# Performance work log

Hardware: AMD Instinct MI355X
Metric: run time of the kernel (lower is better)

Reference implementation:

```python
import jax, jax.numpy as jnp
import numpy as np

B, S, C, HD = 2, 4096, 2048, 128
H = C // HD  # 16 heads
EPS = 1.1920929e-07  # torch RMSNorm default eps for float32 (finfo.eps)


def _make_rope(seq_len, head_dim):
    # Standard RoPE 2x2 rotation matrices: [1, S, 1, head_dim//2, 2, 2]
    half = head_dim // 2
    freqs = 1.0 / (10000.0 ** (np.arange(0, half, dtype=np.float32) / half))
    ang = np.arange(seq_len, dtype=np.float32)[:, None] * freqs[None, :]  # [S, half]
    cos, sin = np.cos(ang), np.sin(ang)
    rot = np.stack([np.stack([cos, -sin], axis=-1),
                    np.stack([sin, cos], axis=-1)], axis=-2)  # [S, half, 2, 2]
    return jnp.asarray(rot[None, :, None])  # [1, S, 1, half, 2, 2]


def setup_inputs() -> dict:
    key = jax.random.key(0)
    ks = jax.random.split(key, 9)
    sc = 1.0 / np.sqrt(C)
    return {
        "x": jax.random.normal(ks[0], (B, S, C), jnp.float32),
        "rope": _make_rope(S, HD),
        "wq": jax.random.normal(ks[1], (C, C), jnp.float32) * sc,
        "bq": jax.random.normal(ks[2], (C,), jnp.float32) * 0.01,
        "wk": jax.random.normal(ks[3], (C, C), jnp.float32) * sc,
        "bk": jax.random.normal(ks[4], (C,), jnp.float32) * 0.01,
        "wv": jax.random.normal(ks[5], (C, C), jnp.float32) * sc,
        "bv": jax.random.normal(ks[6], (C,), jnp.float32) * 0.01,
        "q_norm_w": jnp.ones((HD,), jnp.float32),
        "k_norm_w": jnp.ones((HD,), jnp.float32),
    }


def _rmsnorm(t, w):
    t32 = t.astype(jnp.float32)
    inv = jax.lax.rsqrt(jnp.mean(t32 * t32, axis=-1, keepdims=True) + EPS)
    return (t32 * inv * w).astype(t.dtype)


def _apply_rotary(t, rope):
    # t: [B, S, H, HD] -> pairs [B, S, H, HD//2, 1, 2]; rope: [1, S, 1, HD//2, 2, 2]
    t32 = t.reshape(*t.shape[:-1], HD // 2, 1, 2).astype(jnp.float32)
    out = (rope * t32).sum(axis=-1)  # [B, S, H, HD//2, 2]
    return out.reshape(t.shape).astype(t.dtype)


def reference(x, rope, wq, bq, wk, bk, wv, bv, q_norm_w, k_norm_w):
    # QKV projections (torch Linear: x @ W^T + b)
    q = (jnp.einsum('bsc,oc->bso', x, wq) + bq).reshape(B, S, H, HD)
    k = (jnp.einsum('bsc,oc->bso', x, wk) + bk).reshape(B, S, H, HD)
    v = (jnp.einsum('bsc,oc->bso', x, wv) + bv).reshape(B, S, H, HD)
    # Per-head RMSNorm on q, k (in float32, cast back), then rotary
    q = _apply_rotary(_rmsnorm(q, q_norm_w), rope)
    k = _apply_rotary(_rmsnorm(k, k_norm_w), rope)
    return (q, k, v)
```

## Files before the change

kernel.cpp:

```cpp
#include <hip/hip_runtime.h>


#define M_DIM 8192
#define N_DIM 6144
#define K_DIM 2048
#define NKT 32
#define EPS_RMS 1.1920929e-07f

typedef __bf16 bf16x8 __attribute__((ext_vector_type(8)));
typedef float f32x4 __attribute__((ext_vector_type(4)));

__device__ __forceinline__ void gload16(const void* g, void* l) {
  __builtin_amdgcn_global_load_lds(
      (const __attribute__((address_space(1))) unsigned int*)g,
      (__attribute__((address_space(3))) unsigned int*)l, 16, 0, 0);
}

__device__ __forceinline__ unsigned short f2bf(float f) {
  union { float f; unsigned u; } x; x.f = f;
  unsigned r = x.u + 0x7FFFu + ((x.u >> 16) & 1u);
  return (unsigned short)(r >> 16);
}

__global__ void __launch_bounds__(256) cvt_all(
    const float* __restrict__ x, const float* __restrict__ wq,
    const float* __restrict__ wk, const float* __restrict__ wv,
    unsigned short* __restrict__ xbf, unsigned short* __restrict__ wbf) {
  const int nx4 = M_DIM * K_DIM / 4;
  const int nw4 = K_DIM * K_DIM / 4;
  const int tot = nx4 + 3 * nw4;
  int i = blockIdx.x * blockDim.x + threadIdx.x;
  const int stride = gridDim.x * blockDim.x;
  for (; i < tot; i += stride) {
    const float* s;
    unsigned short* d;
    int j;
    if (i < nx4) { s = x; d = xbf; j = i; }
    else {
      const int k = i - nx4;
      const int sel = k / nw4;
      j = k - sel * nw4;
      s = sel == 0 ? wq : (sel == 1 ? wk : wv);
      d = wbf + (size_t)sel * K_DIM * K_DIM;
    }
    const float4 v = reinterpret_cast<const float4*>(s)[j];
    ushort4 o;
    o.x = f2bf(v.x); o.y = f2bf(v.y); o.z = f2bf(v.z); o.w = f2bf(v.w);
    reinterpret_cast<ushort4*>(d)[j] = o;
  }
}

#define LDS4(ARR, BASE, OFF) (*(const f32x4*)((const char*)(ARR) + (BASE) + (OFF)))

#define MFMA_PH(MH, NH)                                                              \
  {                                                                                  \
    _Pragma("unroll")                                                                \
    for (int mf4 = 0; mf4 < 4; ++mf4) {                                              \
      _Pragma("unroll")                                                              \
      for (int nf2 = 0; nf2 < 2; ++nf2) {                                            \
        f32x4& c = acc[(MH) * 4 + mf4][(NH) * 2 + nf2];                              \
        c = __builtin_amdgcn_mfma_f32_16x16x32_bf16(                                 \
            __builtin_bit_cast(bf16x8, Af[mf4][0]),                                  \
            __builtin_bit_cast(bf16x8, Bf[NH][nf2][0]), c, 0, 0, 0);                 \
        c = __builtin_amdgcn_mfma_f32_16x16x32_bf16(                                 \
            __builtin_bit_cast(bf16x8, Af[mf4][1]),                                  \
            __builtin_bit_cast(bf16x8, Bf[NH][nf2][1]), c, 0, 0, 0);                 \
      }                                                                              \
    }                                                                                \
  }

#define FENCE asm volatile("" ::: "memory")

__global__ void __launch_bounds__(512, 2) gemm_fused(
    const unsigned short* __restrict__ xbf, const unsigned short* __restrict__ wbf,
    const float* __restrict__ rope,
    const float* __restrict__ bq, const float* __restrict__ bk, const float* __restrict__ bv,
    const float* __restrict__ qnw, const float* __restrict__ knw,
    float* __restrict__ dout) {
  const int id = blockIdx.x;
  const int xcd = id & 7;
  const int jb = id >> 3;
  const int bm = (xcd << 2) | (jb & 3);
  const int bn = jb >> 2;
  const int m0 = bm << 8, n0 = bn << 8;
  const int tid = threadIdx.x;
  const int w = tid >> 6, l = tid & 63;
  const int l15 = l & 15, lhi = l >> 4;
  const int wr = w >> 2, wc = w & 3;

  __shared__ __align__(16) unsigned short As[32768];
  __shared__ __align__(16) unsigned short Bs[32768];

  const int srow = tid >> 3;
  const int schunk = (tid & 7) ^ (srow & 7);
  const unsigned short* aSrc = xbf + ((size_t)(m0 + srow) << 11) + (schunk << 3);
  const unsigned short* bSrc = wbf + ((size_t)(n0 + srow) << 11) + (schunk << 3);
  char* aDst = (char*)As + (w << 10);
  char* bDst = (char*)Bs + (w << 10);

#define STA(KT, Q) gload16(aSrc + ((size_t)(Q) << 17) + ((KT) << 6), aDst + ((((KT) & 1) << 15) + ((Q) << 13)))
#define STB(KT, Q) gload16(bSrc + ((size_t)(Q) << 17) + ((KT) << 6), bDst + ((((KT) & 1) << 15) + ((Q) << 13)))

  const int sl0 = ((lhi ^ (l15 & 7)) << 4);
  const int sl1 = (((lhi + 4) ^ (l15 & 7)) << 4);
  unsigned a0 = (wr << 14) + (l15 << 7) + sl0;
  unsigned a1 = (wr << 14) + (l15 << 7) + sl1;
  unsigned b0 = (wc << 13) + (l15 << 7) + sl0;
  unsigned b1 = (wc << 13) + (l15 << 7) + sl1;

  f32x4 acc[8][4];
#pragma unroll
  for (int i = 0; i < 8; ++i)
#pragma unroll
    for (int jj = 0; jj < 4; ++jj) acc[i][jj] = (f32x4){0.f, 0.f, 0.f, 0.f};

  f32x4 Af[4][2];
  f32x4 Bf[2][2][2];

  STA(0, 0); STA(0, 2);
  STB(0, 0); STB(0, 1); STB(0, 2); STB(0, 3);
  STA(0, 1); STA(0, 3);
  asm volatile("s_waitcnt vmcnt(2)" ::: "memory");
  __builtin_amdgcn_s_barrier();
  FENCE;

  for (int kt = 0; kt < NKT; ++kt) {
    const bool notLast = (kt < NKT - 1);
    Af[0][0] = LDS4(As, a0, 0);        Af[0][1] = LDS4(As, a1, 0);
    Bf[0][0][0] = LDS4(Bs, b0, 0);     Bf[0][0][1] = LDS4(Bs, b1, 0);
    Bf[0][1][0] = LDS4(Bs, b0, 2048);  Bf[0][1][1] = LDS4(Bs, b1, 2048);
    Af[1][0] = LDS4(As, a0, 2048);     Af[1][1] = LDS4(As, a1, 2048);
    Af[2][0] = LDS4(As, a0, 4096);     Af[2][1] = LDS4(As, a1, 4096);
    Af[3][0] = LDS4(As, a0, 6144);     Af[3][1] = LDS4(As, a1, 6144);
    Bf[1][0][0] = LDS4(Bs, b0, 4096);  Bf[1][0][1] = LDS4(Bs, b1, 4096);
    Bf[1][1][0] = LDS4(Bs, b0, 6144);  Bf[1][1][1] = LDS4(Bs, b1, 6144);
    if (notLast) {
      STA(kt + 1, 0); STA(kt + 1, 2);
      STB(kt + 1, 0); STB(kt + 1, 1); STB(kt + 1, 2); STB(kt + 1, 3);
    }
    __builtin_amdgcn_s_setprio(1);
    MFMA_PH(0, 0);
    MFMA_PH(0, 1);
    __builtin_amdgcn_s_setprio(0);
    if (notLast) { asm volatile("s_waitcnt vmcnt(6)" ::: "memory"); }
    else         { asm volatile("s_waitcnt vmcnt(0)" ::: "memory"); }
    __builtin_amdgcn_s_barrier();
    FENCE;
    Af[0][0] = LDS4(As, a0, 8192);  Af[0][1] = LDS4(As, a1, 8192);
    Af[1][0] = LDS4(As, a0, 10240); Af[1][1] = LDS4(As, a1, 10240);
    Af[2][0] = LDS4(As, a0, 12288); Af[2][1] = LDS4(As, a1, 12288);
    Af[3][0] = LDS4(As, a0, 14336); Af[3][1] = LDS4(As, a1, 14336);
    if (notLast) { STA(kt + 1, 1); STA(kt + 1, 3); }
    __builtin_amdgcn_s_setprio(1);
    MFMA_PH(1, 0);
    MFMA_PH(1, 1);
    __builtin_amdgcn_s_setprio(0);
    if (notLast) { asm volatile("s_waitcnt vmcnt(2)" ::: "memory"); }
    __builtin_amdgcn_s_barrier();
    FENCE;
    a0 ^= 32768u; a1 ^= 32768u; b0 ^= 32768u; b1 ^= 32768u;
  }

  float* scr = (float*)As;
  const int sec = bn >> 3;
  const int nsec = (n0 & 2047) + (wc << 6);
  const float* bias = sec == 0 ? bq : (sec == 1 ? bk : bv);
  float biasv[4];
#pragma unroll
  for (int nf = 0; nf < 4; ++nf) biasv[nf] = bias[nsec + nf * 16 + l15];
  const size_t outBase = ((size_t)sec << 24);

  if (sec < 2) {
    const float* nwp = sec ? knw : qnw;
    const int colh = (wc & 1) << 6;
    float nwv[4];
#pragma unroll
    for (int nf = 0; nf < 4; ++nf) nwv[nf] = nwp[colh + nf * 16 + l15];
    float ssv[8][4];
#pragma unroll
    for (int mf = 0; mf < 8; ++mf) {
#pragma unroll
      for (int jj = 0; jj < 4; ++jj) {
        float ss = 0.f;
#pragma unroll
        for (int nf = 0; nf < 4; ++nf) {
          const float t = acc[mf][nf][jj] + biasv[nf];
          ss += t * t;
        }
        ss += __shfl_xor(ss, 1);
        ss += __shfl_xor(ss, 2);
        ss += __shfl_xor(ss, 4);
        ss += __shfl_xor(ss, 8);
        ssv[mf][jj] = ss;
      }
    }
    if (l15 == 0) {
#pragma unroll
      for (int mf = 0; mf < 8; ++mf)
#pragma unroll
        for (int jj = 0; jj < 4; ++jj)
          scr[(w << 7) + mf * 16 + (lhi << 2) + jj] = ssv[mf][jj];
    }
    __syncthreads();
#pragma unroll
    for (int mf = 0; mf < 8; ++mf) {
#pragma unroll
      for (int jj = 0; jj < 4; ++jj) {
        const float tot = ssv[mf][jj] + scr[((w ^ 1) << 7) + mf * 16 + (lhi << 2) + jj];
        const float inv = rsqrtf(tot * (1.0f / 128.0f) + EPS_RMS);
        const int m = m0 + (wr << 7) + mf * 16 + (lhi << 2) + jj;
        const float* rp = rope + ((size_t)(m & 4095) << 8);
        float* orow = dout + outBase + ((size_t)m << 11) + nsec + l15;
#pragma unroll
        for (int nf = 0; nf < 4; ++nf) {
          const float tn = (acc[mf][nf][jj] + biasv[nf]) * inv * nwv[nf];
          const float pn = __shfl_xor(tn, 1);
          const int ch = colh + nf * 16 + l15;
          const int jr = ch >> 1;
          const float o = fmaf(rp[jr << 2], tn, rp[(jr << 2) + 1 + (ch & 1)] * pn);
          orow[nf << 4] = o;
        }
      }
    }
  } else {
#pragma unroll
    for (int mf = 0; mf < 8; ++mf)
#pragma unroll
      for (int jj = 0; jj < 4; ++jj) {
        const int m = m0 + (wr << 7) + mf * 16 + (lhi << 2) + jj;
        float* orow = dout + outBase + ((size_t)m << 11) + nsec + l15;
#pragma unroll
        for (int nf = 0; nf < 4; ++nf) orow[nf << 4] = acc[mf][nf][jj] + biasv[nf];
      }
  }
}

extern "C" void kernel_launch(void* const* d_in, const int* in_sizes, int n_in,
                              void* d_out, int out_size, void* d_ws, size_t ws_size,
                              hipStream_t stream) {
  const float* x = (const float*)d_in[0];
  const float* rope = (const float*)d_in[1];
  const float* wq = (const float*)d_in[2];
  const float* bq = (const float*)d_in[3];
  const float* wk = (const float*)d_in[4];
  const float* bk = (const float*)d_in[5];
  const float* wv = (const float*)d_in[6];
  const float* bv = (const float*)d_in[7];
  const float* qnw = (const float*)d_in[8];
  const float* knw = (const float*)d_in[9];

  unsigned short* xbf = (unsigned short*)d_ws;
  unsigned short* wbf = xbf + (size_t)M_DIM * K_DIM;

  cvt_all<<<2048, 256, 0, stream>>>(x, wq, wk, wv, xbf, wbf);

  gemm_fused<<<(M_DIM / 256) * (N_DIM / 256), 512, 0, stream>>>(
      xbf, wbf, rope, bq, bk, bv, qnw, knw, (float*)d_out);
}
```

Measured before the change: 232.5 us.

## Shrink GEMM tile to 128x256 with 4 waves, K-step 32, triple-buffered B

The block tile changes from 256x256 with 8 waves to 128x256 with 4 waves. Each wave now computes the full 128 rows against a 64-column slice, and the K step shrinks from 64 to 32, so the loop runs 64 iterations with one barrier each. B gets three LDS stages and is prefetched two steps ahead, while A stays double-buffered. The LDS swizzle and the block-to-XCD mapping are redone to fit. The smaller tile doubles the block count and cuts LDS use. In exchange, global traffic per FLOP goes up and there are more barrier iterations.

```diff
diff --git a/kernel.cpp b/kernel.cpp
--- a/kernel.cpp
+++ b/kernel.cpp
@@ -4,7 +4,7 @@
 #define M_DIM 8192
 #define N_DIM 6144
 #define K_DIM 2048
-#define NKT 32
+#define NKT2 64
 #define EPS_RMS 1.1920929e-07f
 
 typedef __bf16 bf16x8 __attribute__((ext_vector_type(8)));
@@ -51,27 +51,9 @@
 }
 
 #define LDS4(ARR, BASE, OFF) (*(const f32x4*)((const char*)(ARR) + (BASE) + (OFF)))
-
-#define MFMA_PH(MH, NH)                                                              \
-  {                                                                                  \
-    _Pragma("unroll")                                                                \
-    for (int mf4 = 0; mf4 < 4; ++mf4) {                                              \
-      _Pragma("unroll")                                                              \
-      for (int nf2 = 0; nf2 < 2; ++nf2) {                                            \
-        f32x4& c = acc[(MH) * 4 + mf4][(NH) * 2 + nf2];                              \
-        c = __builtin_amdgcn_mfma_f32_16x16x32_bf16(                                 \
-            __builtin_bit_cast(bf16x8, Af[mf4][0]),                                  \
-            __builtin_bit_cast(bf16x8, Bf[NH][nf2][0]), c, 0, 0, 0);                 \
-        c = __builtin_amdgcn_mfma_f32_16x16x32_bf16(                                 \
-            __builtin_bit_cast(bf16x8, Af[mf4][1]),                                  \
-            __builtin_bit_cast(bf16x8, Bf[NH][nf2][1]), c, 0, 0, 0);                 \
-      }                                                                              \
-    }                                                                                \
-  }
-
 #define FENCE asm volatile("" ::: "memory")
 
-__global__ void __launch_bounds__(512, 2) gemm_fused(
+__global__ void __launch_bounds__(256, 2) gemm_fused(
     const unsigned short* __restrict__ xbf, const unsigned short* __restrict__ wbf,
     const float* __restrict__ rope,
     const float* __restrict__ bq, const float* __restrict__ bk, const float* __restrict__ bv,
@@ -80,33 +62,30 @@
   const int id = blockIdx.x;
   const int xcd = id & 7;
   const int jb = id >> 3;
-  const int bm = (xcd << 2) | (jb & 3);
-  const int bn = jb >> 2;
-  const int m0 = bm << 8, n0 = bn << 8;
+  const int bm = (xcd << 3) | (jb & 7);
+  const int bn = jb >> 3;
+  const int m0 = bm << 7, n0 = bn << 8;
   const int tid = threadIdx.x;
   const int w = tid >> 6, l = tid & 63;
   const int l15 = l & 15, lhi = l >> 4;
-  const int wr = w >> 2, wc = w & 3;
-
-  __shared__ __align__(16) unsigned short As[32768];
-  __shared__ __align__(16) unsigned short Bs[32768];
-
-  const int srow = tid >> 3;
-  const int schunk = (tid & 7) ^ (srow & 7);
-  const unsigned short* aSrc = xbf + ((size_t)(m0 + srow) << 11) + (schunk << 3);
-  const unsigned short* bSrc = wbf + ((size_t)(n0 + srow) << 11) + (schunk << 3);
-  char* aDst = (char*)As + (w << 10);
-  char* bDst = (char*)Bs + (w << 10);
-
-#define STA(KT, Q) gload16(aSrc + ((size_t)(Q) << 17) + ((KT) << 6), aDst + ((((KT) & 1) << 15) + ((Q) << 13)))
-#define STB(KT, Q) gload16(bSrc + ((size_t)(Q) << 17) + ((KT) << 6), bDst + ((((KT) & 1) << 15) + ((Q) << 13)))
-
-  const int sl0 = ((lhi ^ (l15 & 7)) << 4);
-  const int sl1 = (((lhi + 4) ^ (l15 & 7)) << 4);
-  unsigned a0 = (wr << 14) + (l15 << 7) + sl0;
-  unsigned a1 = (wr << 14) + (l15 << 7) + sl1;
-  unsigned b0 = (wc << 13) + (l15 << 7) + sl0;
-  unsigned b1 = (wc << 13) + (l15 << 7) + sl1;
+
+  __shared__ __align__(16) unsigned short As[8192];
+  __shared__ __align__(16) unsigned short Bs[24576];
+
+  const int gchunk = (l & 3) ^ ((l >> 3) & 3);
+  const unsigned short* aSrc = xbf + ((size_t)(m0 + (w << 4) + (l >> 2)) << 11) + (gchunk << 3);
+  const unsigned short* bSrc = wbf + ((size_t)(n0 + (w << 4) + (l >> 2)) << 11) + (gchunk << 3);
+  char* aD = (char*)As + (w << 10);
+  char* bD = (char*)Bs + (w << 10);
+
+#define STA(KT, H) gload16(aSrc + ((size_t)(H) << 17) + ((KT) << 5), \
+                           aD + ((((KT) & 1) << 13) + ((H) << 12)))
+#define STB(KT, Q, BO) gload16(bSrc + ((size_t)(Q) << 17) + ((KT) << 5), \
+                               bD + ((BO) + ((Q) << 12)))
+
+  const int slot = lhi ^ ((l15 >> 1) & 3);
+  const unsigned aRdB = (l15 << 6) + (slot << 4);
+  const unsigned bRdB = (w << 12) + (l15 << 6) + (slot << 4);
 
   f32x4 acc[8][4];
 #pragma unroll
@@ -114,56 +93,51 @@
 #pragma unroll
     for (int jj = 0; jj < 4; ++jj) acc[i][jj] = (f32x4){0.f, 0.f, 0.f, 0.f};
 
-  f32x4 Af[4][2];
-  f32x4 Bf[2][2][2];
-
-  STA(0, 0); STA(0, 2);
-  STB(0, 0); STB(0, 1); STB(0, 2); STB(0, 3);
-  STA(0, 1); STA(0, 3);
-  asm volatile("s_waitcnt vmcnt(2)" ::: "memory");
+  f32x4 Af[8], Bf[4];
+
+  STB(0, 0, 0); STB(0, 1, 0); STB(0, 2, 0); STB(0, 3, 0);
+  STA(0, 0); STA(0, 1);
+  STB(1, 0, 16384); STB(1, 1, 16384); STB(1, 2, 16384); STB(1, 3, 16384);
+  asm volatile("s_waitcnt vmcnt(4)" ::: "memory");
   __builtin_amdgcn_s_barrier();
   FENCE;
 
-  for (int kt = 0; kt < NKT; ++kt) {
-    const bool notLast = (kt < NKT - 1);
-    Af[0][0] = LDS4(As, a0, 0);        Af[0][1] = LDS4(As, a1, 0);
-    Bf[0][0][0] = LDS4(Bs, b0, 0);     Bf[0][0][1] = LDS4(Bs, b1, 0);
-    Bf[0][1][0] = LDS4(Bs, b0, 2048);  Bf[0][1][1] = LDS4(Bs, b1, 2048);
-    Af[1][0] = LDS4(As, a0, 2048);     Af[1][1] = LDS4(As, a1, 2048);
-    Af[2][0] = LDS4(As, a0, 4096);     Af[2][1] = LDS4(As, a1, 4096);
-    Af[3][0] = LDS4(As, a0, 6144);     Af[3][1] = LDS4(As, a1, 6144);
-    Bf[1][0][0] = LDS4(Bs, b0, 4096);  Bf[1][0][1] = LDS4(Bs, b1, 4096);
-    Bf[1][1][0] = LDS4(Bs, b0, 6144);  Bf[1][1][1] = LDS4(Bs, b1, 6144);
-    if (notLast) {
-      STA(kt + 1, 0); STA(kt + 1, 2);
-      STB(kt + 1, 0); STB(kt + 1, 1); STB(kt + 1, 2); STB(kt + 1, 3);
+  unsigned aBuf = 0;
+  unsigned bRB = 0;
+  unsigned bSB = 32768;
+  for (int kt = 0; kt < NKT2; ++kt) {
+    Af[0] = LDS4(As, aBuf + aRdB, 0);    Af[1] = LDS4(As, aBuf + aRdB, 1024);
+    Af[2] = LDS4(As, aBuf + aRdB, 2048); Af[3] = LDS4(As, aBuf + aRdB, 3072);
+    Af[4] = LDS4(As, aBuf + aRdB, 4096); Af[5] = LDS4(As, aBuf + aRdB, 5120);
+    Af[6] = LDS4(As, aBuf + aRdB, 6144); Af[7] = LDS4(As, aBuf + aRdB, 7168);
+    Bf[0] = LDS4(Bs, bRB + bRdB, 0);     Bf[1] = LDS4(Bs, bRB + bRdB, 1024);
+    Bf[2] = LDS4(Bs, bRB + bRdB, 2048);  Bf[3] = LDS4(Bs, bRB + bRdB, 3072);
+    if (kt <= NKT2 - 2) { STA(kt + 1, 0); STA(kt + 1, 1); }
+    if (kt <= NKT2 - 3) {
+      STB(kt + 2, 0, bSB); STB(kt + 2, 1, bSB);
+      STB(kt + 2, 2, bSB); STB(kt + 2, 3, bSB);
     }
     __builtin_amdgcn_s_setprio(1);
-    MFMA_PH(0, 0);
-    MFMA_PH(0, 1);
+#pragma unroll
+    for (int mf = 0; mf < 8; ++mf)
+#pragma unroll
+      for (int nf = 0; nf < 4; ++nf)
+        acc[mf][nf] = __builtin_amdgcn_mfma_f32_16x16x32_bf16(
+            __builtin_bit_cast(bf16x8, Af[mf]),
+            __builtin_bit_cast(bf16x8, Bf[nf]), acc[mf][nf], 0, 0, 0);
     __builtin_amdgcn_s_setprio(0);
-    if (notLast) { asm volatile("s_waitcnt vmcnt(6)" ::: "memory"); }
-    else         { asm volatile("s_waitcnt vmcnt(0)" ::: "memory"); }
+    if (kt <= NKT2 - 3)      { asm volatile("s_waitcnt vmcnt(4)" ::: "memory"); }
+    else if (kt == NKT2 - 2) { asm volatile("s_waitcnt vmcnt(0)" ::: "memory"); }
     __builtin_amdgcn_s_barrier();
     FENCE;
-    Af[0][0] = LDS4(As, a0, 8192);  Af[0][1] = LDS4(As, a1, 8192);
-    Af[1][0] = LDS4(As, a0, 10240); Af[1][1] = LDS4(As, a1, 10240);
-    Af[2][0] = LDS4(As, a0, 12288); Af[2][1] = LDS4(As, a1, 12288);
-    Af[3][0] = LDS4(As, a0, 14336); Af[3][1] = LDS4(As, a1, 14336);
-    if (notLast) { STA(kt + 1, 1); STA(kt + 1, 3); }
-    __builtin_amdgcn_s_setprio(1);
-    MFMA_PH(1, 0);
-    MFMA_PH(1, 1);
-    __builtin_amdgcn_s_setprio(0);
-    if (notLast) { asm volatile("s_waitcnt vmcnt(2)" ::: "memory"); }
-    __builtin_amdgcn_s_barrier();
-    FENCE;
-    a0 ^= 32768u; a1 ^= 32768u; b0 ^= 32768u; b1 ^= 32768u;
+    aBuf ^= 8192u;
+    bRB = (bRB == 32768u) ? 0u : bRB + 16384u;
+    bSB = (bSB == 32768u) ? 0u : bSB + 16384u;
   }
 
   float* scr = (float*)As;
   const int sec = bn >> 3;
-  const int nsec = (n0 & 2047) + (wc << 6);
+  const int nsec = (n0 & 2047) + (w << 6);
   const float* bias = sec == 0 ? bq : (sec == 1 ? bk : bv);
   float biasv[4];
 #pragma unroll
@@ -172,7 +146,7 @@
 
   if (sec < 2) {
     const float* nwp = sec ? knw : qnw;
-    const int colh = (wc & 1) << 6;
+    const int colh = (w & 1) << 6;
     float nwv[4];
 #pragma unroll
     for (int nf = 0; nf < 4; ++nf) nwv[nf] = nwp[colh + nf * 16 + l15];
@@ -208,7 +182,7 @@
       for (int jj = 0; jj < 4; ++jj) {
         const float tot = ssv[mf][jj] + scr[((w ^ 1) << 7) + mf * 16 + (lhi << 2) + jj];
         const float inv = rsqrtf(tot * (1.0f / 128.0f) + EPS_RMS);
-        const int m = m0 + (wr << 7) + mf * 16 + (lhi << 2) + jj;
+        const int m = m0 + mf * 16 + (lhi << 2) + jj;
         const float* rp = rope + ((size_t)(m & 4095) << 8);
         float* orow = dout + outBase + ((size_t)m << 11) + nsec + l15;
 #pragma unroll
@@ -227,7 +201,7 @@
     for (int mf = 0; mf < 8; ++mf)
 #pragma unroll
       for (int jj = 0; jj < 4; ++jj) {
-        const int m = m0 + (wr << 7) + mf * 16 + (lhi << 2) + jj;
+        const int m = m0 + mf * 16 + (lhi << 2) + jj;
         float* orow = dout + outBase + ((size_t)m << 11) + nsec + l15;
 #pragma unroll
         for (int nf = 0; nf < 4; ++nf) orow[nf << 4] = acc[mf][nf][jj] + biasv[nf];
@@ -254,6 +228,6 @@
 
   cvt_all<<<2048, 256, 0, stream>>>(x, wq, wk, wv, xbf, wbf);
 
-  gemm_fused<<<(M_DIM / 256) * (N_DIM / 256), 512, 0, stream>>>(
+  gemm_fused<<<(M_DIM / 128) * (N_DIM / 256), 256, 0, stream>>>(
       xbf, wbf, rope, bq, bk, bv, qnw, knw, (float*)d_out);
 }
```

After: 253.5 us. 1.09x slower.
